# Kernel tuning notes

Hardware: AMD Instinct MI355X
Metric: run time of the kernel (lower is better)

Reference implementation:

```python
import jax, jax.numpy as jnp
import numpy as np
from jax import lax

WINDOW_SIZE = 11
SIGMA = 1.5


def gaussian_window(channel, size=WINDOW_SIZE, sigma=SIGMA):
    coords = jnp.arange(size, dtype=jnp.float32) - size // 2
    g = jnp.exp(-coords ** 2 / (2.0 * sigma ** 2))
    g = g / g.sum()
    w2d = g[:, None] * g[None, :]                       # [size, size]
    return jnp.broadcast_to(w2d, (channel, 1, size, size))  # OIHW, depthwise


def depthwise_conv(x, w, c):
    pad = WINDOW_SIZE // 2
    return lax.conv_general_dilated(
        x, w,
        window_strides=(1, 1),
        padding=[(pad, pad), (pad, pad)],
        dimension_numbers=('NCHW', 'OIHW', 'NCHW'),
        feature_group_count=c,
    )


def setup_inputs() -> dict:
    key = jax.random.key(0)
    k1, k2 = jax.random.split(key)
    pred = jax.random.uniform(k1, (32, 3, 512, 512), dtype=jnp.float32)
    target = jax.random.uniform(k2, (32, 3, 512, 512), dtype=jnp.float32)
    return {"pred": pred, "target": target}


def reference(pred, target):
    c = pred.shape[1]
    w = gaussian_window(c).astype(pred.dtype)
    mu1 = depthwise_conv(pred, w, c)
    mu2 = depthwise_conv(target, w, c)
    mu1_sq = mu1 * mu1
    mu2_sq = mu2 * mu2
    mu1_mu2 = mu1 * mu2
    sigma1_sq = depthwise_conv(pred * pred, w, c) - mu1_sq
    sigma2_sq = depthwise_conv(target * target, w, c) - mu2_sq
    sigma12 = depthwise_conv(pred * target, w, c) - mu1_mu2
    C1 = 0.01 ** 2
    C2 = 0.03 ** 2
    ssim_map = (2.0 * mu1_mu2 + C1) * (2.0 * sigma12 + C2) / (
        (mu1_sq + mu2_sq + C1) * (sigma1_sq + sigma2_sq + C2) + 1e-08)
    return 1.0 - ssim_map.mean()
```

## Files before the change

### kernel.cpp

```cpp
#include <hip/hip_runtime.h>

typedef float f32x2 __attribute__((ext_vector_type(2)));

#define IMG_W 512
#define IMG_H 512
#define TY 8
#define PLANES 96
#define NPIX (32ll * 3 * 512 * 512)
#define NACC 64

#define WG_INIT { 0.00102838f, 0.00759876f, 0.03600077f, 0.10936069f, \
                  0.21300553f, 0.26601172f, 0.21300553f, 0.10936069f, \
                  0.03600077f, 0.00759876f, 0.00102838f }

#define SLAB_ATOMS 272
#define SLAB_BYTES (SLAB_ATOMS * 16)

__device__ __forceinline__ int pmap(int at) {
    const int par = at & 1;
    return (at & ~15) | (par << 3) | (((at >> 1) & 7) ^ (par << 2));
}

__global__ __launch_bounds__(512)
void ssim_main(const float* __restrict__ pred, const float* __restrict__ targ,
               double* __restrict__ acc) {
    const float WG[11] = WG_INIT;

    __shared__ __align__(16) unsigned char ldsraw[8 * SLAB_BYTES];
    __shared__ float wsum[8];

    const int tid   = threadIdx.x;
    const int x     = tid;
    const int plane = blockIdx.y;
    const int y0    = blockIdx.x * TY;
    const size_t base = (size_t)plane * (IMG_W * IMG_H);
    const float* pCol = pred + base + x;
    const float* tCol = targ + base + x;

    if (tid < 64) {
        const int s   = tid >> 3;
        const int idx = tid & 7;
        const int at  = (idx < 4) ? idx : (256 + idx);
        *(float4*)(ldsraw + s * SLAB_BYTES + pmap(at) * 16) =
            (float4){0.f, 0.f, 0.f, 0.f};
    }

    float pv[TY + 10], tv[TY + 10];
#pragma unroll
    for (int iy = 0; iy < TY + 10; ++iy) {
        const int y = y0 - 5 + iy;
        pv[iy] = 0.f; tv[iy] = 0.f;
        if ((unsigned)y < (unsigned)IMG_H) {
            pv[iy] = pCol[(size_t)y * IMG_W];
            tv[iy] = tCol[(size_t)y * IMG_W];
        }
    }

    f32x2 A[4][4];
#pragma unroll
    for (int m = 0; m < 4; ++m)
#pragma unroll
        for (int rp = 0; rp < 4; ++rp) A[m][rp] = (f32x2){0.f, 0.f};

#pragma unroll
    for (int iy = 0; iy < TY + 10; ++iy) {
        const float p = pv[iy], t = tv[iy];
        const float ss = __builtin_fmaf(t, t, p * p);
        const float pt = p * t;
        const f32x2 vs[4] = { {p,p}, {t,t}, {ss,ss}, {pt,pt} };
#pragma unroll
        for (int rp = 0; rp < 4; ++rp) {
            const int a = iy - 2 * rp;
            if (a < 0 || a > 11) continue;
            const float w0 = (a <= 10) ? WG[a] : 0.f;
            const float w1 = (a >= 1)  ? WG[a - 1] : 0.f;
            const f32x2 w = (f32x2){w0, w1};
#pragma unroll
            for (int m = 0; m < 4; ++m)
                A[m][rp] = __builtin_elementwise_fma(vs[m], w, A[m][rp]);
        }
    }

    const int g   = tid & 127;
    const int rpl = tid >> 7;
    const int wat = (x + 8) >> 1;
    const int wof = pmap(wat) * 16 + ((x + 8) & 1) * 8;
    int rof[8];
#pragma unroll
    for (int q = 0; q < 8; ++q) rof[q] = pmap(2 * g + 1 + q) * 16;

    f32x2 H[4][4];
#pragma unroll
    for (int phase = 0; phase < 2; ++phase) {
        if (phase) __syncthreads();
#pragma unroll
        for (int ml = 0; ml < 2; ++ml)
#pragma unroll
            for (int rp = 0; rp < 4; ++rp)
                *(f32x2*)(ldsraw + (ml * 4 + rp) * SLAB_BYTES + wof) =
                    A[phase * 2 + ml][rp];
        __syncthreads();

#pragma unroll
        for (int ml = 0; ml < 2; ++ml) {
            const unsigned char* slab = ldsraw + (ml * 4 + rpl) * SLAB_BYTES;
            f32x2 win[16];
#pragma unroll
            for (int q = 0; q < 8; ++q) {
                const float4 v = *(const float4*)(slab + rof[q]);
                win[2 * q]     = (f32x2){v.x, v.y};
                win[2 * q + 1] = (f32x2){v.z, v.w};
            }
#pragma unroll
            for (int c = 0; c < 4; ++c) {
                f32x2 h = (f32x2){0.f, 0.f};
#pragma unroll
                for (int k = 0; k < 11; ++k) {
                    const f32x2 wk = (f32x2){WG[k], WG[k]};
                    h = __builtin_elementwise_fma(win[c + 1 + k], wk, h);
                }
                H[phase * 2 + ml][c] = h;
            }
        }
    }

    const float C1 = 1e-4f, C2 = 9e-4f;
    float lsum = 0.f;
#pragma unroll
    for (int c = 0; c < 4; ++c) {
        const f32x2 mu1 = H[0][c], mu2 = H[1][c];
        const f32x2 S   = H[2][c], P  = H[3][c];
        const f32x2 mu12 = mu1 * mu2;
        const f32x2 musq = mu1 * mu1 + mu2 * mu2;
        const f32x2 num = (mu12 + mu12 + (f32x2){C1, C1}) *
                          ((P - mu12) + (P - mu12) + (f32x2){C2, C2});
        const f32x2 den = (musq + (f32x2){C1, C1}) *
                          (S - musq + (f32x2){C2, C2}) + (f32x2){1e-8f, 1e-8f};
        lsum += num.x * __builtin_amdgcn_rcpf(den.x);
        lsum += num.y * __builtin_amdgcn_rcpf(den.y);
    }

#pragma unroll
    for (int off = 32; off > 0; off >>= 1)
        lsum += __shfl_down(lsum, off);
    if ((tid & 63) == 0) wsum[tid >> 6] = lsum;
    __syncthreads();
    if (tid == 0) {
        float s = 0.f;
#pragma unroll
        for (int i = 0; i < 8; ++i) s += wsum[i];
        atomicAdd(&acc[blockIdx.x & (NACC - 1)], (double)s);
    }
}

__global__ void ssim_final(const double* __restrict__ acc, float* __restrict__ out) {
    double s = 0.0;
#pragma unroll
    for (int i = 0; i < NACC; ++i) s += acc[i];
    out[0] = 1.0f - (float)(s * (1.0 / (double)NPIX));
}

extern "C" void kernel_launch(void* const* d_in, const int* in_sizes, int n_in,
                              void* d_out, int out_size, void* d_ws, size_t ws_size,
                              hipStream_t stream) {
    const float* pred = (const float*)d_in[0];
    const float* targ = (const float*)d_in[1];
    double* acc = (double*)d_ws;

    hipMemsetAsync(acc, 0, NACC * sizeof(double), stream);

    dim3 grid(IMG_H / TY, PLANES);
    ssim_main<<<grid, 512, 0, stream>>>(pred, targ, acc);
    ssim_final<<<1, 1, 0, stream>>>(acc, (float*)d_out);
}
```

Baseline: 222.6 us.

## Process two columns per thread with 256-thread blocks and float4 LDS stores

```diff
diff --git a/kernel.cpp b/kernel.cpp
--- a/kernel.cpp
+++ b/kernel.cpp
@@ -13,29 +13,26 @@
                   0.21300553f, 0.26601172f, 0.21300553f, 0.10936069f, \
                   0.03600077f, 0.00759876f, 0.00102838f }
 
-#define SLAB_ATOMS 272
+#define SLAB_ATOMS 264
 #define SLAB_BYTES (SLAB_ATOMS * 16)
 
 __device__ __forceinline__ int pmap(int at) {
-    const int par = at & 1;
-    return (at & ~15) | (par << 3) | (((at >> 1) & 7) ^ (par << 2));
+    return (at & ~7) | ((at ^ (at >> 3)) & 7);
 }
 
-__global__ __launch_bounds__(512)
+__global__ __launch_bounds__(256)
 void ssim_main(const float* __restrict__ pred, const float* __restrict__ targ,
                double* __restrict__ acc) {
     const float WG[11] = WG_INIT;
 
     __shared__ __align__(16) unsigned char ldsraw[8 * SLAB_BYTES];
-    __shared__ float wsum[8];
+    __shared__ float wsum[4];
 
     const int tid   = threadIdx.x;
-    const int x     = tid;
+    const int c0    = tid * 2;
     const int plane = blockIdx.y;
     const int y0    = blockIdx.x * TY;
-    const size_t base = (size_t)plane * (IMG_W * IMG_H);
-    const float* pCol = pred + base + x;
-    const float* tCol = targ + base + x;
+    const size_t base = (size_t)plane * (IMG_W * IMG_H) + c0;
 
     if (tid < 64) {
         const int s   = tid >> 3;
@@ -45,74 +42,78 @@
             (float4){0.f, 0.f, 0.f, 0.f};
     }
 
-    float pv[TY + 10], tv[TY + 10];
+    f32x2 A[2][4][4];
+#pragma unroll
+    for (int ch = 0; ch < 2; ++ch)
+#pragma unroll
+        for (int m = 0; m < 4; ++m)
+#pragma unroll
+            for (int rp = 0; rp < 4; ++rp) A[ch][m][rp] = (f32x2){0.f, 0.f};
+
 #pragma unroll
     for (int iy = 0; iy < TY + 10; ++iy) {
         const int y = y0 - 5 + iy;
-        pv[iy] = 0.f; tv[iy] = 0.f;
+        f32x2 p2 = (f32x2){0.f, 0.f}, t2 = (f32x2){0.f, 0.f};
         if ((unsigned)y < (unsigned)IMG_H) {
-            pv[iy] = pCol[(size_t)y * IMG_W];
-            tv[iy] = tCol[(size_t)y * IMG_W];
+            p2 = *(const f32x2*)(pred + base + (size_t)y * IMG_W);
+            t2 = *(const f32x2*)(targ + base + (size_t)y * IMG_W);
+        }
+#pragma unroll
+        for (int ch = 0; ch < 2; ++ch) {
+            const float p = ch ? p2.y : p2.x;
+            const float t = ch ? t2.y : t2.x;
+            const float ss = __builtin_fmaf(t, t, p * p);
+            const float pt = p * t;
+            const f32x2 vs[4] = { {p,p}, {t,t}, {ss,ss}, {pt,pt} };
+#pragma unroll
+            for (int rp = 0; rp < 4; ++rp) {
+                const int a = iy - 2 * rp;
+                if (a < 0 || a > 11) continue;
+                const float w0 = (a <= 10) ? WG[a] : 0.f;
+                const float w1 = (a >= 1)  ? WG[a - 1] : 0.f;
+                const f32x2 w = (f32x2){w0, w1};
+#pragma unroll
+                for (int m = 0; m < 4; ++m)
+                    A[ch][m][rp] =
+                        __builtin_elementwise_fma(vs[m], w, A[ch][m][rp]);
+            }
         }
     }
 
-    f32x2 A[4][4];
+    const int g   = tid & 63;
+    const int rpl = tid >> 6;
+    const int wof = pmap(tid + 4) * 16;
+    int rof[10];
 #pragma unroll
-    for (int m = 0; m < 4; ++m)
-#pragma unroll
-        for (int rp = 0; rp < 4; ++rp) A[m][rp] = (f32x2){0.f, 0.f};
+    for (int q = 0; q < 10; ++q) rof[q] = pmap(4 * g + 1 + q) * 16;
 
-#pragma unroll
-    for (int iy = 0; iy < TY + 10; ++iy) {
-        const float p = pv[iy], t = tv[iy];
-        const float ss = __builtin_fmaf(t, t, p * p);
-        const float pt = p * t;
-        const f32x2 vs[4] = { {p,p}, {t,t}, {ss,ss}, {pt,pt} };
-#pragma unroll
-        for (int rp = 0; rp < 4; ++rp) {
-            const int a = iy - 2 * rp;
-            if (a < 0 || a > 11) continue;
-            const float w0 = (a <= 10) ? WG[a] : 0.f;
-            const float w1 = (a >= 1)  ? WG[a - 1] : 0.f;
-            const f32x2 w = (f32x2){w0, w1};
-#pragma unroll
-            for (int m = 0; m < 4; ++m)
-                A[m][rp] = __builtin_elementwise_fma(vs[m], w, A[m][rp]);
-        }
-    }
-
-    const int g   = tid & 127;
-    const int rpl = tid >> 7;
-    const int wat = (x + 8) >> 1;
-    const int wof = pmap(wat) * 16 + ((x + 8) & 1) * 8;
-    int rof[8];
-#pragma unroll
-    for (int q = 0; q < 8; ++q) rof[q] = pmap(2 * g + 1 + q) * 16;
-
-    f32x2 H[4][4];
+    f32x2 H[4][8];
 #pragma unroll
     for (int phase = 0; phase < 2; ++phase) {
         if (phase) __syncthreads();
 #pragma unroll
         for (int ml = 0; ml < 2; ++ml)
 #pragma unroll
-            for (int rp = 0; rp < 4; ++rp)
-                *(f32x2*)(ldsraw + (ml * 4 + rp) * SLAB_BYTES + wof) =
-                    A[phase * 2 + ml][rp];
+            for (int rp = 0; rp < 4; ++rp) {
+                const int m = phase * 2 + ml;
+                const float4 v = (float4){A[0][m][rp].x, A[0][m][rp].y,
+                                          A[1][m][rp].x, A[1][m][rp].y};
+                *(float4*)(ldsraw + (ml * 4 + rp) * SLAB_BYTES + wof) = v;
+            }
         __syncthreads();
 
 #pragma unroll
         for (int ml = 0; ml < 2; ++ml) {
             const unsigned char* slab = ldsraw + (ml * 4 + rpl) * SLAB_BYTES;
-            f32x2 win[16];
+            f32x2 win[20];
 #pragma unroll
-            for (int q = 0; q < 8; ++q) {
+            for (int q = 0; q < 10; ++q) {
                 const float4 v = *(const float4*)(slab + rof[q]);
                 win[2 * q]     = (f32x2){v.x, v.y};
                 win[2 * q + 1] = (f32x2){v.z, v.w};
             }
 #pragma unroll
-            for (int c = 0; c < 4; ++c) {
+            for (int c = 0; c < 8; ++c) {
                 f32x2 h = (f32x2){0.f, 0.f};
 #pragma unroll
                 for (int k = 0; k < 11; ++k) {
@@ -127,7 +128,7 @@
     const float C1 = 1e-4f, C2 = 9e-4f;
     float lsum = 0.f;
 #pragma unroll
-    for (int c = 0; c < 4; ++c) {
+    for (int c = 0; c < 8; ++c) {
         const f32x2 mu1 = H[0][c], mu2 = H[1][c];
         const f32x2 S   = H[2][c], P  = H[3][c];
         const f32x2 mu12 = mu1 * mu2;
@@ -148,7 +149,7 @@
     if (tid == 0) {
         float s = 0.f;
 #pragma unroll
-        for (int i = 0; i < 8; ++i) s += wsum[i];
+        for (int i = 0; i < 4; ++i) s += wsum[i];
         atomicAdd(&acc[blockIdx.x & (NACC - 1)], (double)s);
     }
 }
@@ -170,6 +171,6 @@
     hipMemsetAsync(acc, 0, NACC * sizeof(double), stream);
 
     dim3 grid(IMG_H / TY, PLANES);
-    ssim_main<<<grid, 512, 0, stream>>>(pred, targ, acc);
+    ssim_main<<<grid, 256, 0, stream>>>(pred, targ, acc);
     ssim_final<<<1, 1, 0, stream>>>(acc, (float*)d_out);
 }
```

Measured after the change: 234.3 us. +5.3%, slower.

## Single-pass LDS staging for all moments and fuse final reduction via last-block

Applied to the files above, without the earlier changes.

```diff
diff --git a/kernel.cpp b/kernel.cpp
--- a/kernel.cpp
+++ b/kernel.cpp
@@ -8,13 +8,16 @@
 #define PLANES 96
 #define NPIX (32ll * 3 * 512 * 512)
 #define NACC 64
+#define NBLOCKS (64 * PLANES)
 
 #define WG_INIT { 0.00102838f, 0.00759876f, 0.03600077f, 0.10936069f, \
                   0.21300553f, 0.26601172f, 0.21300553f, 0.10936069f, \
                   0.03600077f, 0.00759876f, 0.00102838f }
 
-#define SLAB_ATOMS 272
+#define SLAB_ATOMS 256
 #define SLAB_BYTES (SLAB_ATOMS * 16)
+#define NSLABS 16
+#define LDS_TOTAL (NSLABS * SLAB_BYTES)
 
 __device__ __forceinline__ int pmap(int at) {
     const int par = at & 1;
@@ -23,11 +26,10 @@
 
 __global__ __launch_bounds__(512)
 void ssim_main(const float* __restrict__ pred, const float* __restrict__ targ,
-               double* __restrict__ acc) {
+               double* __restrict__ acc, float* __restrict__ out) {
     const float WG[11] = WG_INIT;
 
-    __shared__ __align__(16) unsigned char ldsraw[8 * SLAB_BYTES];
-    __shared__ float wsum[8];
+    __shared__ __align__(16) unsigned char ldsraw[LDS_TOTAL];
 
     const int tid   = threadIdx.x;
     const int x     = tid;
@@ -36,14 +38,6 @@
     const size_t base = (size_t)plane * (IMG_W * IMG_H);
     const float* pCol = pred + base + x;
     const float* tCol = targ + base + x;
-
-    if (tid < 64) {
-        const int s   = tid >> 3;
-        const int idx = tid & 7;
-        const int at  = (idx < 4) ? idx : (256 + idx);
-        *(float4*)(ldsraw + s * SLAB_BYTES + pmap(at) * 16) =
-            (float4){0.f, 0.f, 0.f, 0.f};
-    }
 
     float pv[TY + 10], tv[TY + 10];
 #pragma unroll
@@ -81,47 +75,49 @@
         }
     }
 
+    const int wof = pmap(x >> 1) * 16 + (x & 1) * 8;
+#pragma unroll
+    for (int m = 0; m < 4; ++m)
+#pragma unroll
+        for (int rp = 0; rp < 4; ++rp)
+            *(f32x2*)(ldsraw + (m * 4 + rp) * SLAB_BYTES + wof) = A[m][rp];
+    __syncthreads();
+
     const int g   = tid & 127;
     const int rpl = tid >> 7;
-    const int wat = (x + 8) >> 1;
-    const int wof = pmap(wat) * 16 + ((x + 8) & 1) * 8;
-    int rof[8];
+    int rof[8]; bool msk[8];
 #pragma unroll
-    for (int q = 0; q < 8; ++q) rof[q] = pmap(2 * g + 1 + q) * 16;
+    for (int q = 0; q < 8; ++q) {
+        const int at  = 2 * g - 3 + q;
+        msk[q] = ((unsigned)at <= 255u);
+        const int atc = min(max(at, 0), 255);
+        rof[q] = rpl * SLAB_BYTES + pmap(atc) * 16;
+    }
 
     f32x2 H[4][4];
 #pragma unroll
-    for (int phase = 0; phase < 2; ++phase) {
-        if (phase) __syncthreads();
+    for (int ml = 0; ml < 4; ++ml) {
+        const unsigned char* slab = ldsraw + ml * (4 * SLAB_BYTES);
+        f32x2 win[16];
 #pragma unroll
-        for (int ml = 0; ml < 2; ++ml)
+        for (int q = 0; q < 8; ++q) {
+            float4 v = *(const float4*)(slab + rof[q]);
+            if (!msk[q]) v = (float4){0.f, 0.f, 0.f, 0.f};
+            win[2 * q]     = (f32x2){v.x, v.y};
+            win[2 * q + 1] = (f32x2){v.z, v.w};
+        }
+        f32x2 hacc[4];
 #pragma unroll
-            for (int rp = 0; rp < 4; ++rp)
-                *(f32x2*)(ldsraw + (ml * 4 + rp) * SLAB_BYTES + wof) =
-                    A[phase * 2 + ml][rp];
-        __syncthreads();
-
+        for (int c = 0; c < 4; ++c) hacc[c] = (f32x2){0.f, 0.f};
 #pragma unroll
-        for (int ml = 0; ml < 2; ++ml) {
-            const unsigned char* slab = ldsraw + (ml * 4 + rpl) * SLAB_BYTES;
-            f32x2 win[16];
+        for (int k = 0; k < 11; ++k) {
+            const f32x2 wk = (f32x2){WG[k], WG[k]};
 #pragma unroll
-            for (int q = 0; q < 8; ++q) {
-                const float4 v = *(const float4*)(slab + rof[q]);
-                win[2 * q]     = (f32x2){v.x, v.y};
-                win[2 * q + 1] = (f32x2){v.z, v.w};
-            }
+            for (int c = 0; c < 4; ++c)
+                hacc[c] = __builtin_elementwise_fma(win[c + 1 + k], wk, hacc[c]);
+        }
 #pragma unroll
-            for (int c = 0; c < 4; ++c) {
-                f32x2 h = (f32x2){0.f, 0.f};
-#pragma unroll
-                for (int k = 0; k < 11; ++k) {
-                    const f32x2 wk = (f32x2){WG[k], WG[k]};
-                    h = __builtin_elementwise_fma(win[c + 1 + k], wk, h);
-                }
-                H[phase * 2 + ml][c] = h;
-            }
-        }
+        for (int c = 0; c < 4; ++c) H[ml][c] = hacc[c];
     }
 
     const float C1 = 1e-4f, C2 = 9e-4f;
@@ -140,24 +136,35 @@
         lsum += num.y * __builtin_amdgcn_rcpf(den.y);
     }
 
+    __syncthreads();
+    float*  wsum    = (float*)ldsraw;
+    int*    islastp = (int*)(ldsraw + 64);
 #pragma unroll
     for (int off = 32; off > 0; off >>= 1)
         lsum += __shfl_down(lsum, off);
     if ((tid & 63) == 0) wsum[tid >> 6] = lsum;
     __syncthreads();
+    unsigned int* cnt = (unsigned int*)(acc + NACC);
     if (tid == 0) {
         float s = 0.f;
 #pragma unroll
         for (int i = 0; i < 8; ++i) s += wsum[i];
         atomicAdd(&acc[blockIdx.x & (NACC - 1)], (double)s);
+        __threadfence();
+        const unsigned int old = atomicAdd(cnt, 1u);
+        *islastp = (old == NBLOCKS - 1);
     }
-}
+    __syncthreads();
 
-__global__ void ssim_final(const double* __restrict__ acc, float* __restrict__ out) {
-    double s = 0.0;
+    if (*islastp && tid < 64) {
+        __threadfence();
+        double v = atomicAdd(&acc[tid], 0.0);
 #pragma unroll
-    for (int i = 0; i < NACC; ++i) s += acc[i];
-    out[0] = 1.0f - (float)(s * (1.0 / (double)NPIX));
+        for (int off = 32; off > 0; off >>= 1)
+            v += __shfl_down(v, off);
+        if (tid == 0)
+            out[0] = 1.0f - (float)(v * (1.0 / (double)NPIX));
+    }
 }
 
 extern "C" void kernel_launch(void* const* d_in, const int* in_sizes, int n_in,
@@ -167,9 +174,8 @@
     const float* targ = (const float*)d_in[1];
     double* acc = (double*)d_ws;
 
-    hipMemsetAsync(acc, 0, NACC * sizeof(double), stream);
+    hipMemsetAsync(acc, 0, (NACC + 1) * sizeof(double), stream);
 
     dim3 grid(IMG_H / TY, PLANES);
-    ssim_main<<<grid, 512, 0, stream>>>(pred, targ, acc);
-    ssim_final<<<1, 1, 0, stream>>>(acc, (float*)d_out);
+    ssim_main<<<grid, 512, 0, stream>>>(pred, targ, acc, (float*)d_out);
 }
```

Result: slower. 414.8 us (+86.4%).
